# Performance work log

Measured on AMD Instinct MI355X. Metric: run time of the kernel, lower is better.

Reference implementation:

```python
import jax, jax.numpy as jnp
import numpy as np

L, B, H, IN = 2, 32, 2048, 2048  # layers, batch, hidden, input (=hidden here)


def setup_inputs() -> dict:
    key = jax.random.key(0)
    ks = jax.random.split(key, 8)
    s = 0.02
    return {
        "h0": jax.random.normal(ks[0], (L, B, H), jnp.float32),
        "c0": jax.random.normal(ks[1], (L, B, H), jnp.float32),
        "W_ih": jax.random.normal(ks[2], (L, 4 * H, IN), jnp.float32) * s,
        "W_hh": jax.random.normal(ks[3], (L, 4 * H, H), jnp.float32) * s,
        "b_ih": jax.random.normal(ks[4], (L, 4 * H), jnp.float32) * s,
        "b_hh": jax.random.normal(ks[5], (L, 4 * H), jnp.float32) * s,
        "W_out": jax.random.normal(ks[6], (IN, H), jnp.float32) * s,
        "b_out": jax.random.normal(ks[7], (IN,), jnp.float32) * s,
        "seq_len": 128,
    }


def _lstm_cell(x, h, c, W_ih, W_hh, b_ih, b_hh):
    # gates: [B, 4H]; PyTorch LSTMCell gate order i, f, g, o
    gates = x @ W_ih.T + b_ih + h @ W_hh.T + b_hh
    i, f, g, o = jnp.split(gates, 4, axis=-1)
    c_new = jax.nn.sigmoid(f) * c + jax.nn.sigmoid(i) * jnp.tanh(g)
    h_new = jax.nn.sigmoid(o) * jnp.tanh(c_new)
    return h_new, c_new


def reference(h0, c0, W_ih, W_hh, b_ih, b_hh, W_out, b_out, seq_len):
    batch, hidden = h0.shape[1], h0.shape[2]
    x0 = jnp.zeros((batch, hidden), h0.dtype)

    def step(carry, _):
        x, h, c = carry  # h, c: [L, B, H]
        hs, cs = [], []
        inp = x
        for l in range(h.shape[0]):  # small fixed layer loop
            h_l, c_l = _lstm_cell(inp, h[l], c[l], W_ih[l], W_hh[l], b_ih[l], b_hh[l])
            hs.append(h_l)
            cs.append(c_l)
            inp = h_l
        last_h = hs[-1]
        x_next = last_h @ W_out.T + b_out  # projected feedback
        return (x_next, jnp.stack(hs), jnp.stack(cs)), last_h

    _, out_feats = jax.lax.scan(step, (x0, h0, c0), None, length=seq_len)
    return out_feats  # [seq_len, B, H] (stacked list of per-step top-layer h)
```

## Files before the change

### kernel.cpp

```cpp
#include <hip/hip_runtime.h>


typedef __attribute__((ext_vector_type(8))) short short8;
typedef __attribute__((ext_vector_type(4))) short short4v;
typedef __attribute__((ext_vector_type(4))) float f32x4;

#define MFMA16(a, b, c) __builtin_amdgcn_mfma_f32_16x16x32_bf16((a), (b), (c), 0, 0, 0)

static constexpr int BATCH = 32;
static constexpr int HID = 2048;
static constexpr int NWG = 256;
static constexpr int NTHR = 512;
static constexpr int BH = BATCH * HID;
static constexpr size_t WMAT = (size_t)8192 * 2048;
static constexpr int LDS_RED_OFF = 139264;
static constexpr int LDS_BYTES = 155648;

__device__ __forceinline__ unsigned short f2bf(float x) {
  unsigned u = __float_as_uint(x);
  u += 0x7FFFu + ((u >> 16) & 1u);
  return (unsigned short)(u >> 16);
}
__device__ __forceinline__ float sigm(float x) { return 1.f / (1.f + __expf(-x)); }
__device__ __forceinline__ float tanh_(float x) {
  float e = __expf(2.f * x);
  return 1.f - 2.f / (e + 1.f);
}

__global__ void cvt_bf16_k(const float* __restrict__ s, unsigned short* __restrict__ d,
                           long n4) {
  long i = blockIdx.x * (long)blockDim.x + threadIdx.x;
  long st = (long)gridDim.x * blockDim.x;
  for (; i < n4; i += st) {
    float4 v = ((const float4*)s)[i];
    short4v o;
    o.x = (short)f2bf(v.x); o.y = (short)f2bf(v.y);
    o.z = (short)f2bf(v.z); o.w = (short)f2bf(v.w);
    ((short4v*)d)[i] = o;
  }
}

__global__ void tcvt_k(const float* __restrict__ src, unsigned short* __restrict__ dst) {
  __shared__ float T[64][65];
  const int jb = blockIdx.x * 64, kb = blockIdx.y * 64;
  const int tid = threadIdx.x;
#pragma unroll
  for (int r = 0; r < 4; ++r) {
    const int row = r * 16 + (tid >> 4), c4 = (tid & 15) * 4;
    float4 v = *(const float4*)&src[(size_t)(jb + row) * 2048 + kb + c4];
    T[row][c4] = v.x; T[row][c4 + 1] = v.y; T[row][c4 + 2] = v.z; T[row][c4 + 3] = v.w;
  }
  __syncthreads();
#pragma unroll
  for (int r = 0; r < 4; ++r) {
    const int k = r * 16 + (tid >> 4), j4 = (tid & 15) * 4;
    short4v o;
    o.x = (short)f2bf(T[j4][k]);     o.y = (short)f2bf(T[j4 + 1][k]);
    o.z = (short)f2bf(T[j4 + 2][k]); o.w = (short)f2bf(T[j4 + 3][k]);
    *(short4v*)&dst[(size_t)(kb + k) * 2048 + jb + j4] = o;
  }
}

__global__ void gemm_pack_k(const unsigned short* __restrict__ A,
                            const unsigned short* __restrict__ Bt,
                            unsigned short* __restrict__ Wfp) {
  __shared__ __align__(16) unsigned short As[128][72], Bs[128][72];
  const int tid = threadIdx.x, wv = tid >> 6, lane = tid & 63;
  const int wm = wv >> 1, wn = wv & 1;
  const int g0 = blockIdx.x * 128, k0 = blockIdx.y * 128;
  f32x4 acc[4][4];
#pragma unroll
  for (int i = 0; i < 4; ++i)
#pragma unroll
    for (int j = 0; j < 4; ++j) acc[i][j] = (f32x4){0.f, 0.f, 0.f, 0.f};

  for (int kt = 0; kt < 32; ++kt) {
#pragma unroll
    for (int rr = 0; rr < 4; ++rr) {
      const int row = rr * 32 + (tid >> 3), c8 = (tid & 7) * 8;
      *(short8*)&As[row][c8] = *(const short8*)&A[(size_t)(g0 + row) * 2048 + kt * 64 + c8];
      *(short8*)&Bs[row][c8] = *(const short8*)&Bt[(size_t)(k0 + row) * 2048 + kt * 64 + c8];
    }
    __syncthreads();
#pragma unroll
    for (int kk = 0; kk < 2; ++kk) {
      short8 af[4], bf[4];
#pragma unroll
      for (int mi = 0; mi < 4; ++mi)
        af[mi] = *(const short8*)&As[wm * 64 + mi * 16 + (lane & 15)][kk * 32 + (lane >> 4) * 8];
#pragma unroll
      for (int ni = 0; ni < 4; ++ni)
        bf[ni] = *(const short8*)&Bs[wn * 64 + ni * 16 + (lane & 15)][kk * 32 + (lane >> 4) * 8];
#pragma unroll
      for (int mi = 0; mi < 4; ++mi)
#pragma unroll
        for (int ni = 0; ni < 4; ++ni)
          acc[mi][ni] = MFMA16(af[mi], bf[ni], acc[mi][ni]);
    }
    __syncthreads();
  }
#pragma unroll
  for (int mi = 0; mi < 4; ++mi)
#pragma unroll
    for (int ni = 0; ni < 4; ++ni)
#pragma unroll
      for (int r = 0; r < 4; ++r) {
        const int g = g0 + wm * 64 + mi * 16 + (lane >> 4) * 4 + r;
        const int k = k0 + wn * 64 + ni * 16 + (lane & 15);
        const int gateblk = g >> 11, gcol = g & 2047;
        const int wgp = gcol >> 3, nn = (gcol & 7) + 8 * (gateblk & 1), tile = gateblk >> 1;
        const int kblk = k >> 5, e = k & 7, lane_p = nn + 16 * ((k >> 3) & 3);
        Wfp[(((size_t)(wgp * 2 + tile) * 64 + kblk) * 64 + lane_p) * 8 + e] =
            f2bf(acc[mi][ni][r]);
      }
}

__global__ void pack_W1_k(const float* __restrict__ src, unsigned short* __restrict__ dst) {
  const int bid = blockIdx.x;
  const int wg = bid >> 1, tile = bid & 1;
  const int tid = threadIdx.x;
  __shared__ __align__(16) unsigned short L[16][2056];
  for (int i = tid; i < 16 * 512; i += 256) {
    const int r = i >> 9, c4 = i & 511;
    const int gr = tile * 4096 + (r < 8 ? wg * 8 + r : 2048 + wg * 8 + r - 8);
    float4 v = ((const float4*)(src + (size_t)gr * 2048))[c4];
    short4v o;
    o.x = (short)f2bf(v.x); o.y = (short)f2bf(v.y);
    o.z = (short)f2bf(v.z); o.w = (short)f2bf(v.w);
    *(short4v*)&L[r][c4 * 4] = o;
  }
  __syncthreads();
  short8* dchunks = (short8*)dst;
  const size_t cbase = (size_t)(wg * 2 + tile) * 64;
  for (int c = tid; c < 4096; c += 256) {
    const int lane = c & 63, kblk = c >> 6;
    const int nn = lane & 15, kb = (lane >> 4) << 3;
    short8 v = *(const short8*)&L[nn][kblk * 32 + kb];
    dchunks[(cbase + kblk) * 64 + lane] = v;
  }
}

__global__ void bias_k(const float* __restrict__ Wih, const float* __restrict__ bout,
                       const float* __restrict__ bih, const float* __restrict__ bhh,
                       float* bA0, float* bAf, float* bB) {
  const int g = blockIdx.x * 8 + (threadIdx.x >> 6);
  const int lane = threadIdx.x & 63;
  float s = 0.f;
  for (int i = 0; i < 32; ++i)
    s += Wih[(size_t)g * 2048 + i * 64 + lane] * bout[i * 64 + lane];
  for (int off = 32; off; off >>= 1) s += __shfl_down(s, off);
  if (lane == 0) {
    const float b0 = bih[g] + bhh[g];
    bA0[g] = b0; bAf[g] = b0 + s;
    bB[g] = bih[8192 + g] + bhh[8192 + g];
  }
}

__global__ void init_k(const float* __restrict__ h0, const float* __restrict__ c0,
                       unsigned short* h0p, unsigned short* h1p, unsigned short* zbuf,
                       float* c0f, float* c1f, unsigned* bar) {
  int i = blockIdx.x * blockDim.x + threadIdx.x;
  if (i < BH) {
    const int e = i & 7, lane = (i >> 3) & 63, kblk = (i >> 9) & 63, mtile = i >> 15;
    const int m = mtile * 16 + (lane & 15);
    const int k = kblk * 32 + ((lane >> 4) << 3) + e;
    h0p[i] = f2bf(h0[m * HID + k]);
    h1p[i] = f2bf(h0[BH + m * HID + k]);
    zbuf[i] = 0;
    c0f[i] = c0[i];
    c1f[i] = c0[BH + i];
  }
  if (i < 320) bar[i] = 0u;
}

__device__ __forceinline__ void grid_barrier(unsigned* bar, int bno) {
  __syncthreads();
  if (threadIdx.x == 0) {
    __builtin_amdgcn_fence(__ATOMIC_RELEASE, "agent");
    const int g = blockIdx.x >> 5;
    unsigned a = __hip_atomic_fetch_add(&bar[g * 32], 1u,
                                        __ATOMIC_RELAXED, __HIP_MEMORY_SCOPE_AGENT);
    if (a == (unsigned)(32 * bno - 1)) {
      unsigned m = __hip_atomic_fetch_add(&bar[256], 1u,
                                          __ATOMIC_RELAXED, __HIP_MEMORY_SCOPE_AGENT);
      if (m == (unsigned)(8 * bno - 1)) {
        __hip_atomic_store(&bar[288], (unsigned)bno,
                           __ATOMIC_RELAXED, __HIP_MEMORY_SCOPE_AGENT);
      }
    }
    while (__hip_atomic_load(&bar[288], __ATOMIC_RELAXED,
                             __HIP_MEMORY_SCOPE_AGENT) < (unsigned)bno) {
      __builtin_amdgcn_s_sleep(2);
    }
    __builtin_amdgcn_fence(__ATOMIC_ACQUIRE, "agent");
  }
  __syncthreads();
}

#define PHASE_BODY(VARR, NV2, LBASE, CBUF, HOUTP, OUTP, BSEL)                     \
  {                                                                               \
    const short8* pa0 = (const short8*)Asrc + (size_t)(ks * 16) * 64 + lane;      \
    const short8* pa1 = pa0 + (size_t)64 * 64;                                    \
    f32x4 acc00 = {0.f, 0.f, 0.f, 0.f}, acc01 = acc00, acc10 = acc00, acc11 = acc00; \
    _Pragma("unroll")                                                             \
    for (int kk = 0; kk < NV2; ++kk) {                                            \
      short8 a0 = pa0[kk * 64], a1 = pa1[kk * 64];                                \
      short8 b0 = VARR[kk], b1 = VARR[16 + kk];                                   \
      acc00 = MFMA16(a0, b0, acc00); acc01 = MFMA16(a1, b0, acc01);               \
      acc10 = MFMA16(a0, b1, acc10); acc11 = MFMA16(a1, b1, acc11);               \
    }                                                                             \
    _Pragma("unroll")                                                             \
    for (int kk = NV2; kk < 16; ++kk) {                                           \
      short8 a0 = pa0[kk * 64], a1 = pa1[kk * 64];                                \
      short8 b0 = VARR[kk];                                                       \
      short8 b1 = lw[(w * 17 + LBASE + (kk - NV2)) * 64 + lane];                  \
      acc00 = MFMA16(a0, b0, acc00); acc01 = MFMA16(a1, b0, acc01);               \
      acc10 = MFMA16(a0, b1, acc10); acc11 = MFMA16(a1, b1, acc11);               \
    }                                                                             \
    *(f32x4*)&red[((w * 2 + 0) * 64 + lane) * 4] = acc00;                         \
    *(f32x4*)&red[((w * 2 + 1) * 64 + lane) * 4] = acc01;                         \
    __syncthreads();                                                              \
    float gi = 0.f, gf_ = 0.f;                                                    \
    if (tid < 256) {                                                              \
      const int b = tid >> 3, cc = tid & 7, m = b >> 4, br = b & 15;              \
      const int reg = br & 3, lb = (br >> 2) << 4;                                \
      _Pragma("unroll")                                                           \
      for (int ww = 0; ww < 8; ++ww) {                                            \
        gi  += red[((ww * 2 + m) * 64 + lb + cc) * 4 + reg];                      \
        gf_ += red[((ww * 2 + m) * 64 + lb + cc + 8) * 4 + reg];                  \
      }                                                                           \
    }                                                                             \
    __syncthreads();                                                              \
    *(f32x4*)&red[((w * 2 + 0) * 64 + lane) * 4] = acc10;                         \
    *(f32x4*)&red[((w * 2 + 1) * 64 + lane) * 4] = acc11;                         \
    __syncthreads();                                                              \
    if (tid < 256) {                                                              \
      const int b = tid >> 3, cc = tid & 7, m = b >> 4, br = b & 15;              \
      const int reg = br & 3, lb = (br >> 2) << 4;                                \
      float gg = 0.f, go = 0.f;                                                   \
      _Pragma("unroll")                                                           \
      for (int ww = 0; ww < 8; ++ww) {                                            \
        gg += red[((ww * 2 + m) * 64 + lb + cc) * 4 + reg];                       \
        go += red[((ww * 2 + m) * 64 + lb + cc + 8) * 4 + reg];                   \
      }                                                                           \
      const int col = wg * 8 + cc;                                                \
      gi  += (BSEL)[col];                                                         \
      gf_ += (BSEL)[2048 + col];                                                  \
      gg  += (BSEL)[4096 + col];                                                  \
      go  += (BSEL)[6144 + col];                                                  \
      const float iv = sigm(gi), fv = sigm(gf_), gv = tanh_(gg), ov = sigm(go);   \
      const float cold = (CBUF)[b * HID + col];                                   \
      const float cnew = fv * cold + iv * gv;                                     \
      const float hnew = ov * tanh_(cnew);                                        \
      (CBUF)[b * HID + col] = cnew;                                               \
      const int kblk = col >> 5, lh = (col >> 3) & 3, e = col & 7;                \
      const int lane_p = (b & 15) | (lh << 4), mt = b >> 4;                       \
      (HOUTP)[((size_t)(mt * 64 + kblk) * 64 + lane_p) * 8 + e] = f2bf(hnew);     \
      if (OUTP) ((float*)(OUTP))[b * HID + col] = hnew;                           \
    }                                                                             \
  }

__global__ __launch_bounds__(NTHR, 1) void lstm_persist(
    const unsigned short* __restrict__ Wfp, const unsigned short* __restrict__ Wh0p,
    const unsigned short* __restrict__ Wi1p, const unsigned short* __restrict__ Wh1p,
    const float* __restrict__ bA0, const float* __restrict__ bAf,
    const float* __restrict__ bB,
    unsigned short* h0p, unsigned short* h1p, const unsigned short* zbuf,
    float* c0f, float* c1f, float* __restrict__ out, int T, unsigned* bar) {
  extern __shared__ __align__(16) char smem[];
  short8* lw = (short8*)smem;
  float* red = (float*)(smem + LDS_RED_OFF);
  const int wg = blockIdx.x, tid = threadIdx.x;
  const int w = tid >> 6, lane = tid & 63, ks = w & 3;
  const unsigned short* M0 = (w < 4) ? Wfp : Wh0p;
  const unsigned short* M1 = (w < 4) ? Wi1p : Wh1p;

  short8 v0[24], v1[23];
  {
    const short8* m0c = (const short8*)M0;
    const short8* m1c = (const short8*)M1;
#pragma unroll
    for (int c = 0; c < 24; ++c)
      v0[c] = m0c[(((size_t)(wg * 2 + (c >> 4)) * 64) + ks * 16 + (c & 15)) * 64 + lane];
#pragma unroll
    for (int c = 24; c < 32; ++c)
      lw[(w * 17 + (c - 24)) * 64 + lane] =
          m0c[(((size_t)(wg * 2 + (c >> 4)) * 64) + ks * 16 + (c & 15)) * 64 + lane];
#pragma unroll
    for (int c = 0; c < 23; ++c)
      v1[c] = m1c[(((size_t)(wg * 2 + (c >> 4)) * 64) + ks * 16 + (c & 15)) * 64 + lane];
#pragma unroll
    for (int c = 23; c < 32; ++c)
      lw[(w * 17 + 8 + (c - 23)) * 64 + lane] =
          m1c[(((size_t)(wg * 2 + (c >> 4)) * 64) + ks * 16 + (c & 15)) * 64 + lane];
  }
  __syncthreads();

  int bno = 1;
  for (int t = 0; t < T; ++t) {
    const int par = t & 1;
    {
      const unsigned short* Asrc =
          (w < 4) ? ((t == 0) ? zbuf : h1p + par * BH) : (h0p + par * BH);
      const float* bsel = (t == 0) ? bA0 : bAf;
      PHASE_BODY(v0, 8, 0, c0f, h0p + (par ^ 1) * BH, (float*)nullptr, bsel)
    }
    grid_barrier(bar, bno++);
    {
      const unsigned short* Asrc = (w < 4) ? (h0p + (par ^ 1) * BH) : (h1p + par * BH);
      PHASE_BODY(v1, 7, 8, c1f, h1p + (par ^ 1) * BH, out + (size_t)t * BH, bB)
    }
    grid_barrier(bar, bno++);
  }
}

extern "C" void kernel_launch(void* const* d_in, const int* in_sizes, int n_in,
                              void* d_out, int out_size, void* d_ws, size_t ws_size,
                              hipStream_t stream) {
  const float* h0 = (const float*)d_in[0];
  const float* c0 = (const float*)d_in[1];
  const float* Wih = (const float*)d_in[2];
  const float* Whh = (const float*)d_in[3];
  const float* bih = (const float*)d_in[4];
  const float* bhh = (const float*)d_in[5];
  const float* Wout = (const float*)d_in[6];
  const float* bout = (const float*)d_in[7];
  float* out = (float*)d_out;
  const int T = out_size / BH;

  unsigned short* Wfp = (unsigned short*)d_ws;
  unsigned short* Wh0p = Wfp + WMAT;
  unsigned short* Wi1p = Wfp + 2 * WMAT;
  unsigned short* Wh1p = Wfp + 3 * WMAT;
  unsigned short* tmpA = Wi1p;
  unsigned short* WoutT = Wh1p;
  unsigned short* S = Wfp + 4 * WMAT;
  unsigned short* h0p = S;
  unsigned short* h1p = S + 131072;
  unsigned short* zbuf = S + 262144;
  float* F = (float*)(S + 327680);
  float* c0f = F;
  float* c1f = F + 65536;
  float* bA0 = F + 131072;
  float* bAf = F + 139264;
  float* bB = F + 147456;
  unsigned* bar = (unsigned*)(F + 155648);

  cvt_bf16_k<<<2048, 256, 0, stream>>>(Wih, tmpA, (long)(WMAT / 4));
  tcvt_k<<<dim3(32, 32), 256, 0, stream>>>(Wout, WoutT);
  gemm_pack_k<<<dim3(64, 16), 256, 0, stream>>>(tmpA, WoutT, Wfp);
  pack_W1_k<<<512, 256, 0, stream>>>(Whh, Wh0p);
  pack_W1_k<<<512, 256, 0, stream>>>(Wih + WMAT, Wi1p);
  pack_W1_k<<<512, 256, 0, stream>>>(Whh + WMAT, Wh1p);
  bias_k<<<1024, 512, 0, stream>>>(Wih, bout, bih, bhh, bA0, bAf, bB);
  init_k<<<256, 256, 0, stream>>>(h0, c0, h0p, h1p, zbuf, c0f, c1f, bar);

  (void)hipFuncSetAttribute((const void*)lstm_persist,
                            hipFuncAttributeMaxDynamicSharedMemorySize, LDS_BYTES);
  lstm_persist<<<NWG, NTHR, LDS_BYTES, stream>>>(Wfp, Wh0p, Wi1p, Wh1p,
                                                 bA0, bAf, bB,
                                                 h0p, h1p, zbuf, c0f, c1f, out, T, bar);
}
```

Measured before the change: 3.725 ms.

## Replicate hidden state per XCD with two-stage barrier and local copy

Hidden-state writes now bypass caches into a global staging buffer. After the grid barrier, a subset of workgroups on each XCD copies that buffer into an XCD-private replica, followed by a second per-XCD barrier. Later MFMA reads then hit the local L2 replica instead of crossing XCDs. The cost is an extra copy and an extra barrier per phase, plus explicit cache invalidations, and the code relies on reading the hardware XCC id register.

```diff
diff --git a/kernel.cpp b/kernel.cpp
--- a/kernel.cpp
+++ b/kernel.cpp
@@ -4,6 +4,7 @@
 typedef __attribute__((ext_vector_type(8))) short short8;
 typedef __attribute__((ext_vector_type(4))) short short4v;
 typedef __attribute__((ext_vector_type(4))) float f32x4;
+typedef __attribute__((ext_vector_type(4))) unsigned int u32x4;
 
 #define MFMA16(a, b, c) __builtin_amdgcn_mfma_f32_16x16x32_bf16((a), (b), (c), 0, 0, 0)
 
@@ -15,6 +16,10 @@
 static constexpr size_t WMAT = (size_t)8192 * 2048;
 static constexpr int LDS_RED_OFF = 139264;
 static constexpr int LDS_BYTES = 155648;
+
+#define AT_ADD(p, v) __hip_atomic_fetch_add((p), (v), __ATOMIC_RELAXED, __HIP_MEMORY_SCOPE_AGENT)
+#define AT_LD(p) __hip_atomic_load((p), __ATOMIC_RELAXED, __HIP_MEMORY_SCOPE_AGENT)
+#define AT_ST(p, v) __hip_atomic_store((p), (v), __ATOMIC_RELAXED, __HIP_MEMORY_SCOPE_AGENT)
 
 __device__ __forceinline__ unsigned short f2bf(float x) {
   unsigned u = __float_as_uint(x);
@@ -157,44 +162,63 @@
 }
 
 __global__ void init_k(const float* __restrict__ h0, const float* __restrict__ c0,
-                       unsigned short* h0p, unsigned short* h1p, unsigned short* zbuf,
-                       float* c0f, float* c1f, unsigned* bar) {
+                       unsigned short* hX, unsigned short* zbuf,
+                       float* c0f, float* c1f, unsigned* ctl) {
   int i = blockIdx.x * blockDim.x + threadIdx.x;
   if (i < BH) {
     const int e = i & 7, lane = (i >> 3) & 63, kblk = (i >> 9) & 63, mtile = i >> 15;
     const int m = mtile * 16 + (lane & 15);
     const int k = kblk * 32 + ((lane >> 4) << 3) + e;
-    h0p[i] = f2bf(h0[m * HID + k]);
-    h1p[i] = f2bf(h0[BH + m * HID + k]);
+    const unsigned short v0 = f2bf(h0[m * HID + k]);
+    const unsigned short v1 = f2bf(h0[BH + m * HID + k]);
+#pragma unroll
+    for (int x = 0; x < 8; ++x) {
+      hX[(size_t)x * 131072 + i] = v0;
+      hX[(size_t)x * 131072 + 65536 + i] = v1;
+    }
     zbuf[i] = 0;
     c0f[i] = c0[i];
     c1f[i] = c0[BH + i];
   }
-  if (i < 320) bar[i] = 0u;
-}
-
-__device__ __forceinline__ void grid_barrier(unsigned* bar, int bno) {
+  if (i < 832) ctl[i] = 0u;
+}
+
+__device__ __forceinline__ void phase_sync(unsigned* ctl, int bno, int lbno, int xcc,
+                                           int role, int n_x, int n_c, int w, int lane,
+                                           const unsigned short* hGm,
+                                           unsigned short* Xm) {
+  asm volatile("s_waitcnt vmcnt(0)" ::: "memory");
   __syncthreads();
   if (threadIdx.x == 0) {
-    __builtin_amdgcn_fence(__ATOMIC_RELEASE, "agent");
     const int g = blockIdx.x >> 5;
-    unsigned a = __hip_atomic_fetch_add(&bar[g * 32], 1u,
-                                        __ATOMIC_RELAXED, __HIP_MEMORY_SCOPE_AGENT);
+    unsigned a = AT_ADD(&ctl[g * 32], 1u);
     if (a == (unsigned)(32 * bno - 1)) {
-      unsigned m = __hip_atomic_fetch_add(&bar[256], 1u,
-                                          __ATOMIC_RELAXED, __HIP_MEMORY_SCOPE_AGENT);
-      if (m == (unsigned)(8 * bno - 1)) {
-        __hip_atomic_store(&bar[288], (unsigned)bno,
-                           __ATOMIC_RELAXED, __HIP_MEMORY_SCOPE_AGENT);
-      }
-    }
-    while (__hip_atomic_load(&bar[288], __ATOMIC_RELAXED,
-                             __HIP_MEMORY_SCOPE_AGENT) < (unsigned)bno) {
-      __builtin_amdgcn_s_sleep(2);
-    }
-    __builtin_amdgcn_fence(__ATOMIC_ACQUIRE, "agent");
-  }
-  __syncthreads();
+      unsigned m = AT_ADD(&ctl[256], 1u);
+      if (m == (unsigned)(8 * bno - 1)) AT_ST(&ctl[288], (unsigned)bno);
+    }
+    while (AT_LD(&ctl[288]) < (unsigned)bno) __builtin_amdgcn_s_sleep(1);
+  }
+  __syncthreads();
+  asm volatile("buffer_inv" ::: "memory");
+  if (role < n_c) {
+    for (int c = role * 8 + w; c < 128; c += n_c * 8) {
+      const unsigned short* s = hGm + c * 512 + lane * 8;
+      u32x4 v;
+      asm volatile("global_load_dwordx4 %0, %1, off sc0 sc1"
+                   : "=v"(v) : "v"((unsigned long long)(size_t)s) : "memory");
+      asm volatile("s_waitcnt vmcnt(0)" ::: "memory");
+      *(u32x4*)(Xm + c * 512 + lane * 8) = v;
+    }
+  }
+  asm volatile("s_waitcnt vmcnt(0)" ::: "memory");
+  __syncthreads();
+  if (threadIdx.x == 0) {
+    AT_ADD(&ctl[320 + xcc * 32], 1u);
+    while (AT_LD(&ctl[320 + xcc * 32]) < (unsigned)(n_x * lbno))
+      __builtin_amdgcn_s_sleep(1);
+  }
+  __syncthreads();
+  asm volatile("buffer_inv" ::: "memory");
 }
 
 #define PHASE_BODY(VARR, NV2, LBASE, CBUF, HOUTP, OUTP, BSEL)                     \
@@ -255,7 +279,11 @@
       (CBUF)[b * HID + col] = cnew;                                               \
       const int kblk = col >> 5, lh = (col >> 3) & 3, e = col & 7;                \
       const int lane_p = (b & 15) | (lh << 4), mt = b >> 4;                       \
-      (HOUTP)[((size_t)(mt * 64 + kblk) * 64 + lane_p) * 8 + e] = f2bf(hnew);     \
+      const unsigned hv = (unsigned)f2bf(hnew);                                   \
+      unsigned long long ha = (unsigned long long)(size_t)                        \
+          ((HOUTP) + ((size_t)(mt * 64 + kblk) * 64 + lane_p) * 8 + e);           \
+      asm volatile("global_store_short %0, %1, off sc0 sc1"                       \
+                   :: "v"(ha), "v"(hv) : "memory");                               \
       if (OUTP) ((float*)(OUTP))[b * HID + col] = hnew;                           \
     }                                                                             \
   }
@@ -265,15 +293,20 @@
     const unsigned short* __restrict__ Wi1p, const unsigned short* __restrict__ Wh1p,
     const float* __restrict__ bA0, const float* __restrict__ bAf,
     const float* __restrict__ bB,
-    unsigned short* h0p, unsigned short* h1p, const unsigned short* zbuf,
-    float* c0f, float* c1f, float* __restrict__ out, int T, unsigned* bar) {
+    unsigned short* hX,
+    unsigned short* hG,
+    const unsigned short* zbuf,
+    float* c0f, float* c1f, float* __restrict__ out, int T, unsigned* ctl) {
   extern __shared__ __align__(16) char smem[];
   short8* lw = (short8*)smem;
   float* red = (float*)(smem + LDS_RED_OFF);
   const int wg = blockIdx.x, tid = threadIdx.x;
   const int w = tid >> 6, lane = tid & 63, ks = w & 3;
+  const int xcc = (int)(__builtin_amdgcn_s_getreg((20) | (0 << 6) | (31 << 11)) & 7);
   const unsigned short* M0 = (w < 4) ? Wfp : Wh0p;
   const unsigned short* M1 = (w < 4) ? Wi1p : Wh1p;
+
+  if (tid == 0) *(int*)red = (int)AT_ADD(&ctl[576 + xcc * 32], 1u);
 
   short8 v0[24], v1[23];
   {
@@ -295,22 +328,40 @@
           m1c[(((size_t)(wg * 2 + (c >> 4)) * 64) + ks * 16 + (c & 15)) * 64 + lane];
   }
   __syncthreads();
-
-  int bno = 1;
+  const int role = *(int*)red;
+  unsigned short* Xh0 = hX + (size_t)xcc * 131072;
+  unsigned short* Xh1 = Xh0 + 65536;
+
+  asm volatile("s_waitcnt vmcnt(0)" ::: "memory");
+  __syncthreads();
+  if (tid == 0) {
+    const int g = blockIdx.x >> 5;
+    unsigned a = AT_ADD(&ctl[g * 32], 1u);
+    if (a == 31u) {
+      unsigned m = AT_ADD(&ctl[256], 1u);
+      if (m == 7u) AT_ST(&ctl[288], 1u);
+    }
+    while (AT_LD(&ctl[288]) < 1u) __builtin_amdgcn_s_sleep(1);
+    *(int*)red = (int)AT_LD(&ctl[576 + xcc * 32]);
+  }
+  __syncthreads();
+  const int n_x = *(int*)red;
+  const int n_c = n_x < 16 ? n_x : 16;
+  __syncthreads();
+
+  int bno = 2, lbno = 1;
   for (int t = 0; t < T; ++t) {
-    const int par = t & 1;
     {
-      const unsigned short* Asrc =
-          (w < 4) ? ((t == 0) ? zbuf : h1p + par * BH) : (h0p + par * BH);
+      const unsigned short* Asrc = (w < 4) ? ((t == 0) ? zbuf : Xh1) : Xh0;
       const float* bsel = (t == 0) ? bA0 : bAf;
-      PHASE_BODY(v0, 8, 0, c0f, h0p + (par ^ 1) * BH, (float*)nullptr, bsel)
-    }
-    grid_barrier(bar, bno++);
+      PHASE_BODY(v0, 8, 0, c0f, hG, (float*)nullptr, bsel)
+    }
+    phase_sync(ctl, bno++, lbno++, xcc, role, n_x, n_c, w, lane, hG, Xh0);
     {
-      const unsigned short* Asrc = (w < 4) ? (h0p + (par ^ 1) * BH) : (h1p + par * BH);
-      PHASE_BODY(v1, 7, 8, c1f, h1p + (par ^ 1) * BH, out + (size_t)t * BH, bB)
-    }
-    grid_barrier(bar, bno++);
+      const unsigned short* Asrc = (w < 4) ? Xh0 : Xh1;
+      PHASE_BODY(v1, 7, 8, c1f, hG + 65536, out + (size_t)t * BH, bB)
+    }
+    phase_sync(ctl, bno++, lbno++, xcc, role, n_x, n_c, w, lane, hG + 65536, Xh1);
   }
 }
 
@@ -335,16 +386,16 @@
   unsigned short* tmpA = Wi1p;
   unsigned short* WoutT = Wh1p;
   unsigned short* S = Wfp + 4 * WMAT;
-  unsigned short* h0p = S;
-  unsigned short* h1p = S + 131072;
-  unsigned short* zbuf = S + 262144;
-  float* F = (float*)(S + 327680);
+  unsigned short* hX = S;
+  unsigned short* hG = S + 1048576;
+  unsigned short* zbuf = S + 1179648;
+  float* F = (float*)(S + 1245184);
   float* c0f = F;
   float* c1f = F + 65536;
   float* bA0 = F + 131072;
   float* bAf = F + 139264;
   float* bB = F + 147456;
-  unsigned* bar = (unsigned*)(F + 155648);
+  unsigned* ctl = (unsigned*)(F + 155648);
 
   cvt_bf16_k<<<2048, 256, 0, stream>>>(Wih, tmpA, (long)(WMAT / 4));
   tcvt_k<<<dim3(32, 32), 256, 0, stream>>>(Wout, WoutT);
@@ -353,11 +404,11 @@
   pack_W1_k<<<512, 256, 0, stream>>>(Wih + WMAT, Wi1p);
   pack_W1_k<<<512, 256, 0, stream>>>(Whh + WMAT, Wh1p);
   bias_k<<<1024, 512, 0, stream>>>(Wih, bout, bih, bhh, bA0, bAf, bB);
-  init_k<<<256, 256, 0, stream>>>(h0, c0, h0p, h1p, zbuf, c0f, c1f, bar);
+  init_k<<<256, 256, 0, stream>>>(h0, c0, hX, zbuf, c0f, c1f, ctl);
 
   (void)hipFuncSetAttribute((const void*)lstm_persist,
                             hipFuncAttributeMaxDynamicSharedMemorySize, LDS_BYTES);
   lstm_persist<<<NWG, NTHR, LDS_BYTES, stream>>>(Wfp, Wh0p, Wi1p, Wh1p,
                                                  bA0, bAf, bB,
-                                                 h0p, h1p, zbuf, c0f, c1f, out, T, bar);
-}
+                                                 hX, hG, zbuf, c0f, c1f, out, T, ctl);
+}
```

New measurement: 3.682 ms. About the same (-1.2%).

## Stream half of weights per step via async global-to-LDS ring buffers

Applied to the files above, without the earlier changes.

Instead of keeping all weight fragments resident in registers and LDS, each wave now keeps half of its weights in registers and streams the other half from global memory every phase. It uses global_load_lds DMA into per-wave LDS rings, with the activation tiles prefetched the same way. A four-deep pipeline with explicit vmcnt waits overlaps the loads with the MFMAs. This reduces register and LDS pressure, and launch bounds now allow two blocks per CU. The cost is re-reading half the weights from L2/HBM on every timestep.

```diff
diff --git a/kernel.cpp b/kernel.cpp
--- a/kernel.cpp
+++ b/kernel.cpp
@@ -6,6 +6,10 @@
 typedef __attribute__((ext_vector_type(4))) float f32x4;
 
 #define MFMA16(a, b, c) __builtin_amdgcn_mfma_f32_16x16x32_bf16((a), (b), (c), 0, 0, 0)
+#define GDMA(gp, lp)                                                        \
+  __builtin_amdgcn_global_load_lds(                                         \
+      (const __attribute__((address_space(1))) unsigned int*)(gp),          \
+      (__attribute__((address_space(3))) unsigned int*)(lp), 16, 0, 0)
 
 static constexpr int BATCH = 32;
 static constexpr int HID = 2048;
@@ -13,8 +17,14 @@
 static constexpr int NTHR = 512;
 static constexpr int BH = BATCH * HID;
 static constexpr size_t WMAT = (size_t)8192 * 2048;
-static constexpr int LDS_RED_OFF = 139264;
-static constexpr int LDS_BYTES = 155648;
+static constexpr int LDS_WRING = 0;
+static constexpr int LDS_ARING = 32768;
+static constexpr int LDS_RED = 98304;
+static constexpr int LDS_BYTES = 114688;
+
+#define AT_ADD(p, v) __hip_atomic_fetch_add((p), (v), __ATOMIC_RELAXED, __HIP_MEMORY_SCOPE_AGENT)
+#define AT_LD(p) __hip_atomic_load((p), __ATOMIC_RELAXED, __HIP_MEMORY_SCOPE_AGENT)
+#define AT_ST(p, v) __hip_atomic_store((p), (v), __ATOMIC_RELAXED, __HIP_MEMORY_SCOPE_AGENT)
 
 __device__ __forceinline__ unsigned short f2bf(float x) {
   unsigned u = __float_as_uint(x);
@@ -174,49 +184,55 @@
 }
 
 __device__ __forceinline__ void grid_barrier(unsigned* bar, int bno) {
+  asm volatile("s_waitcnt vmcnt(0)" ::: "memory");
   __syncthreads();
   if (threadIdx.x == 0) {
     __builtin_amdgcn_fence(__ATOMIC_RELEASE, "agent");
     const int g = blockIdx.x >> 5;
-    unsigned a = __hip_atomic_fetch_add(&bar[g * 32], 1u,
-                                        __ATOMIC_RELAXED, __HIP_MEMORY_SCOPE_AGENT);
+    unsigned a = AT_ADD(&bar[g * 32], 1u);
     if (a == (unsigned)(32 * bno - 1)) {
-      unsigned m = __hip_atomic_fetch_add(&bar[256], 1u,
-                                          __ATOMIC_RELAXED, __HIP_MEMORY_SCOPE_AGENT);
-      if (m == (unsigned)(8 * bno - 1)) {
-        __hip_atomic_store(&bar[288], (unsigned)bno,
-                           __ATOMIC_RELAXED, __HIP_MEMORY_SCOPE_AGENT);
-      }
-    }
-    while (__hip_atomic_load(&bar[288], __ATOMIC_RELAXED,
-                             __HIP_MEMORY_SCOPE_AGENT) < (unsigned)bno) {
-      __builtin_amdgcn_s_sleep(2);
-    }
+      unsigned m = AT_ADD(&bar[256], 1u);
+      if (m == (unsigned)(8 * bno - 1)) AT_ST(&bar[288], (unsigned)bno);
+    }
+    while (AT_LD(&bar[288]) < (unsigned)bno) __builtin_amdgcn_s_sleep(2);
     __builtin_amdgcn_fence(__ATOMIC_ACQUIRE, "agent");
   }
   __syncthreads();
 }
 
-#define PHASE_BODY(VARR, NV2, LBASE, CBUF, HOUTP, OUTP, BSEL)                     \
+#define PHASE(VARR, WMATP, CBUF, HOUTP, OUTP, BSEL)                               \
   {                                                                               \
-    const short8* pa0 = (const short8*)Asrc + (size_t)(ks * 16) * 64 + lane;      \
-    const short8* pa1 = pa0 + (size_t)64 * 64;                                    \
+    const char* Ab = (const char*)Asrc + ((size_t)(s * 16)) * 1024 + lane * 16;   \
+    const char* Wb = (const char*)(WMATP) +                                       \
+                     (((size_t)(wg * 2 + 1) * 64) + s * 16) * 1024 + lane * 16;   \
+    _Pragma("unroll")                                                             \
+    for (int g = 0; g < 4; ++g) {                                                 \
+      GDMA(Ab + (size_t)g * 1024,         lds3 + aring + g * 2048);               \
+      GDMA(Ab + 65536 + (size_t)g * 1024, lds3 + aring + g * 2048 + 1024);        \
+      GDMA(Wb + (size_t)g * 1024,         lds3 + wring + g * 1024);               \
+    }                                                                             \
     f32x4 acc00 = {0.f, 0.f, 0.f, 0.f}, acc01 = acc00, acc10 = acc00, acc11 = acc00; \
     _Pragma("unroll")                                                             \
-    for (int kk = 0; kk < NV2; ++kk) {                                            \
-      short8 a0 = pa0[kk * 64], a1 = pa1[kk * 64];                                \
-      short8 b0 = VARR[kk], b1 = VARR[16 + kk];                                   \
+    for (int k = 0; k < 16; ++k) {                                                \
+      if (k <= 12)      { asm volatile("s_waitcnt vmcnt(9)" ::: "memory"); }      \
+      else if (k == 13) { asm volatile("s_waitcnt vmcnt(6)" ::: "memory"); }      \
+      else if (k == 14) { asm volatile("s_waitcnt vmcnt(3)" ::: "memory"); }      \
+      else              { asm volatile("s_waitcnt vmcnt(0)" ::: "memory"); }      \
+      __builtin_amdgcn_sched_barrier(0);                                          \
+      short8 a0 = *(const short8*)(smem + aring + (k & 3) * 2048 + lane * 16);    \
+      short8 a1 = *(const short8*)(smem + aring + (k & 3) * 2048 + 1024 + lane * 16); \
+      short8 b1 = *(const short8*)(smem + wring + (k & 3) * 1024 + lane * 16);    \
+      short8 b0 = VARR[k];                                                        \
       acc00 = MFMA16(a0, b0, acc00); acc01 = MFMA16(a1, b0, acc01);               \
       acc10 = MFMA16(a0, b1, acc10); acc11 = MFMA16(a1, b1, acc11);               \
+      __builtin_amdgcn_sched_barrier(0);                                          \
+      if (k < 12) {                                                               \
+        GDMA(Ab + (size_t)(k + 4) * 1024,         lds3 + aring + ((k + 4) & 3) * 2048); \
+        GDMA(Ab + 65536 + (size_t)(k + 4) * 1024, lds3 + aring + ((k + 4) & 3) * 2048 + 1024); \
+        GDMA(Wb + (size_t)(k + 4) * 1024,         lds3 + wring + ((k + 4) & 3) * 1024); \
+      }                                                                           \
     }                                                                             \
-    _Pragma("unroll")                                                             \
-    for (int kk = NV2; kk < 16; ++kk) {                                           \
-      short8 a0 = pa0[kk * 64], a1 = pa1[kk * 64];                                \
-      short8 b0 = VARR[kk];                                                       \
-      short8 b1 = lw[(w * 17 + LBASE + (kk - NV2)) * 64 + lane];                  \
-      acc00 = MFMA16(a0, b0, acc00); acc01 = MFMA16(a1, b0, acc01);               \
-      acc10 = MFMA16(a0, b1, acc10); acc11 = MFMA16(a1, b1, acc11);               \
-    }                                                                             \
+    __syncthreads();                                                              \
     *(f32x4*)&red[((w * 2 + 0) * 64 + lane) * 4] = acc00;                         \
     *(f32x4*)&red[((w * 2 + 1) * 64 + lane) * 4] = acc01;                         \
     __syncthreads();                                                              \
@@ -260,7 +276,7 @@
     }                                                                             \
   }
 
-__global__ __launch_bounds__(NTHR, 1) void lstm_persist(
+__global__ __launch_bounds__(NTHR, 2) void lstm_persist(
     const unsigned short* __restrict__ Wfp, const unsigned short* __restrict__ Wh0p,
     const unsigned short* __restrict__ Wi1p, const unsigned short* __restrict__ Wh1p,
     const float* __restrict__ bA0, const float* __restrict__ bAf,
@@ -268,47 +284,48 @@
     unsigned short* h0p, unsigned short* h1p, const unsigned short* zbuf,
     float* c0f, float* c1f, float* __restrict__ out, int T, unsigned* bar) {
   extern __shared__ __align__(16) char smem[];
-  short8* lw = (short8*)smem;
-  float* red = (float*)(smem + LDS_RED_OFF);
+  auto* lds3 = (__attribute__((address_space(3))) char*)smem;
+  float* red = (float*)(smem + LDS_RED);
   const int wg = blockIdx.x, tid = threadIdx.x;
-  const int w = tid >> 6, lane = tid & 63, ks = w & 3;
-  const unsigned short* M0 = (w < 4) ? Wfp : Wh0p;
-  const unsigned short* M1 = (w < 4) ? Wi1p : Wh1p;
-
-  short8 v0[24], v1[23];
+  const int w = tid >> 6, lane = tid & 63;
+  const int p = w >> 2, s = w & 3;
+  const int wring = LDS_WRING + w * 4096;
+  const int aring = LDS_ARING + w * 8192;
+  const unsigned short* M0 = p ? Wh0p : Wfp;
+  const unsigned short* M1 = p ? Wh1p : Wi1p;
+
+  short8 vA[16], vB[16];
   {
     const short8* m0c = (const short8*)M0;
     const short8* m1c = (const short8*)M1;
 #pragma unroll
-    for (int c = 0; c < 24; ++c)
-      v0[c] = m0c[(((size_t)(wg * 2 + (c >> 4)) * 64) + ks * 16 + (c & 15)) * 64 + lane];
-#pragma unroll
-    for (int c = 24; c < 32; ++c)
-      lw[(w * 17 + (c - 24)) * 64 + lane] =
-          m0c[(((size_t)(wg * 2 + (c >> 4)) * 64) + ks * 16 + (c & 15)) * 64 + lane];
-#pragma unroll
-    for (int c = 0; c < 23; ++c)
-      v1[c] = m1c[(((size_t)(wg * 2 + (c >> 4)) * 64) + ks * 16 + (c & 15)) * 64 + lane];
-#pragma unroll
-    for (int c = 23; c < 32; ++c)
-      lw[(w * 17 + 8 + (c - 23)) * 64 + lane] =
-          m1c[(((size_t)(wg * 2 + (c >> 4)) * 64) + ks * 16 + (c & 15)) * 64 + lane];
-  }
-  __syncthreads();
+    for (int c = 0; c < 16; ++c)
+      vA[c] = m0c[(((size_t)(wg * 2 + 0) * 64) + s * 16 + c) * 64 + lane];
+#pragma unroll
+    for (int c = 0; c < 16; ++c)
+      vB[c] = m1c[(((size_t)(wg * 2 + 0) * 64) + s * 16 + c) * 64 + lane];
+  }
+#pragma unroll
+  for (int c = 0; c < 16; ++c) {
+    asm volatile("" : "+v"(vA[c]));
+    asm volatile("" : "+v"(vB[c]));
+  }
+  asm volatile("s_waitcnt vmcnt(0)" ::: "memory");
+  __builtin_amdgcn_sched_barrier(0);
 
   int bno = 1;
   for (int t = 0; t < T; ++t) {
     const int par = t & 1;
     {
       const unsigned short* Asrc =
-          (w < 4) ? ((t == 0) ? zbuf : h1p + par * BH) : (h0p + par * BH);
+          (p == 0) ? ((t == 0) ? zbuf : h1p + par * BH) : (h0p + par * BH);
       const float* bsel = (t == 0) ? bA0 : bAf;
-      PHASE_BODY(v0, 8, 0, c0f, h0p + (par ^ 1) * BH, (float*)nullptr, bsel)
+      PHASE(vA, M0, c0f, h0p + (par ^ 1) * BH, (float*)nullptr, bsel)
     }
     grid_barrier(bar, bno++);
     {
-      const unsigned short* Asrc = (w < 4) ? (h0p + (par ^ 1) * BH) : (h1p + par * BH);
-      PHASE_BODY(v1, 7, 8, c1f, h1p + (par ^ 1) * BH, out + (size_t)t * BH, bB)
+      const unsigned short* Asrc = (p == 0) ? (h0p + (par ^ 1) * BH) : (h1p + par * BH);
+      PHASE(vB, M1, c1f, h1p + (par ^ 1) * BH, out + (size_t)t * BH, bB)
     }
     grid_barrier(bar, bno++);
   }
```

New measurement: 4.321 ms. 16.0% more time.
